# Performance work log

Hardware: AMD Instinct MI355X
Metric: run time of the kernel (lower is better)

## Reference

```python
import jax, jax.numpy as jnp
import numpy as np

N = 10000          # total nodes
N_AGENTS = 5000    # drones (x[:, -1] < 0)
E = 160000         # random edges (self-loops added in reference)
C_IN, H, C_HID, C_OUT = 16, 8, 128, 8
NEG_SLOPE = 0.2    # GATv2Conv default leaky_relu slope


def setup_inputs() -> dict:
    key = jax.random.key(0)
    ks = jax.random.split(key, 12)
    x = jax.random.normal(ks[0], (N, C_IN), dtype=jnp.float32)
    # last feature column encodes node type: <0 -> drone, >=0 -> goal
    type_col = jnp.where(jnp.arange(N) < N_AGENTS, -1.0, 1.0).astype(jnp.float32)
    x = x.at[:, -1].set(type_col)
    edge_index = jax.random.randint(ks[1], (2, E), 0, N, dtype=jnp.int32)
    s = 0.1  # glorot-ish scale
    return {
        "x": x,
        "edge_index": edge_index,
        "Wl1": s * jax.random.normal(ks[2], (C_IN, H * C_HID), jnp.float32),
        "bl1": jnp.zeros((H * C_HID,), jnp.float32),
        "Wr1": s * jax.random.normal(ks[3], (C_IN, H * C_HID), jnp.float32),
        "br1": jnp.zeros((H * C_HID,), jnp.float32),
        "att1": s * jax.random.normal(ks[4], (H, C_HID), jnp.float32),
        "b1": jnp.zeros((C_HID,), jnp.float32),
        "Wl2": s * jax.random.normal(ks[5], (C_HID, H * C_HID), jnp.float32),
        "bl2": jnp.zeros((H * C_HID,), jnp.float32),
        "Wr2": s * jax.random.normal(ks[6], (C_HID, H * C_HID), jnp.float32),
        "br2": jnp.zeros((H * C_HID,), jnp.float32),
        "att2": s * jax.random.normal(ks[7], (H, C_HID), jnp.float32),
        "b2": jnp.zeros((C_HID,), jnp.float32),
        "Wlin": s * jax.random.normal(ks[8], (C_HID, C_OUT), jnp.float32),
        "blin": jnp.zeros((C_OUT,), jnp.float32),
    }


def gatv2_conv(x, src, dst, Wl, bl, Wr, br, att, bias):
    """PyG GATv2Conv, heads=H, concat=False (head-mean), add_self_loops handled by caller."""
    n = x.shape[0]
    xl = (x @ Wl + bl).reshape(n, H, -1)   # [N,H,C] source transform
    xr = (x @ Wr + br).reshape(n, H, -1)   # [N,H,C] target transform
    e = jax.nn.leaky_relu(xl[src] + xr[dst], NEG_SLOPE)          # [E,H,C]
    alpha = jnp.einsum("ehc,hc->eh", e, att)                      # [E,H]
    # per-destination softmax over incoming edges
    m = jax.ops.segment_max(alpha, dst, num_segments=n)
    a = jnp.exp(alpha - m[dst])
    denom = jax.ops.segment_sum(a, dst, num_segments=n)
    a = a / (denom[dst] + 1e-16)
    out = jax.ops.segment_sum(xl[src] * a[:, :, None], dst, num_segments=n)  # [N,H,C]
    return out.mean(axis=1) + bias  # concat=False -> mean over heads


def reference(x, edge_index, Wl1, bl1, Wr1, br1, att1, b1,
              Wl2, bl2, Wr2, br2, att2, b2, Wlin, blin):
    n = x.shape[0]
    loops = jnp.arange(n, dtype=edge_index.dtype)
    src = jnp.concatenate([edge_index[0], loops])
    dst = jnp.concatenate([edge_index[1], loops])
    drone_mask = x[:, -1] < 0
    y = x  # bounds is None -> no division
    h = jax.nn.relu(gatv2_conv(y, src, dst, Wl1, bl1, Wr1, br1, att1, b1))
    h = jax.nn.relu(gatv2_conv(h, src, dst, Wl2, bl2, Wr2, br2, att2, b2))
    out = h @ Wlin + blin  # [N, C_OUT]
    idx = jnp.nonzero(drone_mask, size=N_AGENTS)[0]
    return out[idx]  # [N_AGENTS, C_OUT]
```

## Files before the change

kernel.cpp:

```cpp
#include <hip/hip_runtime.h>
#include <hip/hip_fp16.h>
#include <math.h>

#define N_NODES 10000
#define N_EDGES 160000
#define NAG     5000
#define HC      1024
#define CH      128
#define NEG     0.2f
#define BCAP    64

#define NSCAT   625
#define NGEMM   1256

typedef _Float16 f16x8 __attribute__((ext_vector_type(8)));
typedef _Float16 f16x2 __attribute__((ext_vector_type(2)));
typedef float f32x4 __attribute__((ext_vector_type(4)));

__device__ __forceinline__ __half2 pk_max(__half2 a, __half2 b) {
    __half2 r;
    asm volatile("v_pk_max_f16 %0, %1, %2" : "=v"(r) : "v"(a), "v"(b));
    return r;
}

__device__ __forceinline__ void edge_accum(float4 raw, const __half2* xr2, const __half2* att2,
                                           float& lsum, float* acc, bool valid) {
    __half2* hp = (__half2*)&raw;
    const __half2 neg2 = __float2half2_rn(NEG);
    float p = 0.f;
    #pragma unroll
    for (int j = 0; j < 4; j++) {
        __half2 z = __hadd2(hp[j], xr2[j]);
        __half2 lz = pk_max(z, __hmul2(z, neg2));
#if __has_builtin(__builtin_amdgcn_fdot2)
        p = __builtin_amdgcn_fdot2(*(f16x2*)&lz, *(const f16x2*)&att2[j], p, false);
#else
        float2 lf = __half22float2(lz);
        float2 af = __half22float2(att2[j]);
        p = fmaf(lf.x, af.x, p);
        p = fmaf(lf.y, af.y, p);
#endif
    }
    p += __shfl_xor(p, 1, 64);
    p += __shfl_xor(p, 2, 64);
    p += __shfl_xor(p, 4, 64);
    p += __shfl_xor(p, 8, 64);
    float w = valid ? __expf(p) : 0.f;
    lsum += w;
    #pragma unroll
    for (int j = 0; j < 4; j++) {
        acc[2 * j]     = fmaf(__low2float(hp[j]),  w, acc[2 * j]);
        acc[2 * j + 1] = fmaf(__high2float(hp[j]), w, acc[2 * j + 1]);
    }
}

template <int K, int KA, bool TRANS, typename AT>
__device__ void gemm_tile(char* smem, int vt,
                          const AT* __restrict__ A, const float* __restrict__ tb,
                          const _Float16* __restrict__ Whl, const float* __restrict__ bl,
                          const _Float16* __restrict__ Whr, const float* __restrict__ br,
                          _Float16* __restrict__ xl, _Float16* __restrict__ xr,
                          int limitL, int limitR) {
    _Float16* ash = (_Float16*)smem;
    float (*eps)[68] = (float(*)[68])smem;
    __shared__ float bsh[256];
    const int AS = K + 8;
    int by = vt & 7;
    int rowblk = (vt >> 3) * 64;
    bool right = by >= 4;
    if (rowblk >= (right ? limitR : limitL)) return;
    const _Float16* Wh = right ? Whr : Whl;
    const float* bs    = right ? br : bl;
    _Float16* outp     = right ? xr : xl;
    int colbase = (by & 3) * 256;
    int t = threadIdx.x;
    int w = t >> 6, l = t & 63;
    int m = l & 15, q = l >> 4;

    bsh[t] = bs[colbase + t];
    for (int idx = t; idx < 64 * (K / 8); idx += 256) {
        int r  = idx / (K / 8);
        int c8 = (idx % (K / 8)) * 8;
        int row = rowblk + r;
        f16x8 hv = (f16x8){0, 0, 0, 0, 0, 0, 0, 0};
        if (row < N_NODES && c8 < KA) {
            if constexpr (TRANS) {
                f16x8 hvv[8];
                #pragma unroll
                for (int h = 0; h < 8; h++)
                    hvv[h] = *(const f16x8*)((const _Float16*)A + (size_t)row * HC + h * CH + c8);
                #pragma unroll
                for (int j = 0; j < 8; j++) {
                    float s = 0.f;
                    #pragma unroll
                    for (int h = 0; h < 8; h++) s += (float)hvv[h][j];
                    hv[j] = (_Float16)fmaxf(fmaf(s, 0.125f, tb[c8 + j]), 0.f);
                }
            } else if constexpr (sizeof(AT) == 2) {
                hv = *(const f16x8*)((const _Float16*)A + (size_t)row * KA + c8);
            } else {
                float4 v0 = *(const float4*)((const float*)A + (size_t)row * KA + c8);
                float4 v1 = *(const float4*)((const float*)A + (size_t)row * KA + c8 + 4);
                hv[0] = (_Float16)v0.x; hv[1] = (_Float16)v0.y; hv[2] = (_Float16)v0.z; hv[3] = (_Float16)v0.w;
                hv[4] = (_Float16)v1.x; hv[5] = (_Float16)v1.y; hv[6] = (_Float16)v1.z; hv[7] = (_Float16)v1.w;
            }
        }
        *(f16x8*)&ash[r * AS + c8] = hv;
    }
    __syncthreads();

    f32x4 acc[16];
    #pragma unroll
    for (int i = 0; i < 16; i++) acc[i] = (f32x4){0.f, 0.f, 0.f, 0.f};

    #pragma unroll
    for (int kq = 0; kq < K / 32; kq++) {
        f16x8 af = *(const f16x8*)&ash[(w * 16 + m) * AS + kq * 32 + q * 8];
        const _Float16* base = Wh + (((size_t)(kq * 64 + (colbase >> 4))) << 9) + l * 8;
        #pragma unroll
        for (int tile = 0; tile < 16; tile++) {
            f16x8 bf = *(const f16x8*)(base + ((size_t)tile << 9));
            acc[tile] = __builtin_amdgcn_mfma_f32_16x16x32_f16(af, bf, acc[tile], 0, 0, 0);
        }
    }

    float bv[16];
    #pragma unroll
    for (int tile = 0; tile < 16; tile++) bv[tile] = bsh[tile * 16 + m];

    for (int cgk = 0; cgk < 4; cgk++) {
        __syncthreads();
        #pragma unroll
        for (int tt = 0; tt < 4; tt++) {
            int tile = cgk * 4 + tt;
            int cl = tt * 16 + m;
            #pragma unroll
            for (int reg = 0; reg < 4; reg++)
                eps[w * 16 + q * 4 + reg][cl] = acc[tile][reg] + bv[tile];
        }
        __syncthreads();
        int colg = colbase + cgk * 64;
        int cc = (t & 15) * 4;
        #pragma unroll
        for (int it = 0; it < 4; it++) {
            int r = it * 16 + (t >> 4);
            int row = rowblk + r;
            if (row < N_NODES) {
                float4 v = *(const float4*)&eps[r][cc];
                __half2 h01 = __floats2half2_rn(v.x, v.y);
                __half2 h23 = __floats2half2_rn(v.z, v.w);
                float2 st;
                st.x = *(float*)&h01;
                st.y = *(float*)&h23;
                *(float2*)(outp + (size_t)row * HC + colg + cc) = st;
            }
        }
    }
}

__global__ __launch_bounds__(64) void gat_kernel(const __half* __restrict__ xl,
                                                 const _Float16* __restrict__ xr,
                                                 const float* __restrict__ att,
                                                 const int* __restrict__ cnt,
                                                 const int* __restrict__ srcs,
                                                 _Float16* __restrict__ hpart) {
    int b = blockIdx.x;
    int dst = b >> 3, head = b & 7;
    int t = threadIdx.x;
    int slot = t >> 4, l16 = t & 15;
    int ch0 = head * CH + l16 * 8;

    __half2 xr2[4], att2[4];
    {
        f16x8 xv = *(const f16x8*)(xr + (size_t)dst * HC + ch0);
        __half2* xp = (__half2*)&xv;
        xr2[0] = xp[0]; xr2[1] = xp[1]; xr2[2] = xp[2]; xr2[3] = xp[3];
        float4 b0 = *(const float4*)(att + ch0);
        float4 b1 = *(const float4*)(att + ch0 + 4);
        att2[0] = __floats2half2_rn(b0.x, b0.y);
        att2[1] = __floats2half2_rn(b0.z, b0.w);
        att2[2] = __floats2half2_rn(b1.x, b1.y);
        att2[3] = __floats2half2_rn(b1.z, b1.w);
    }

    float acc[8];
    #pragma unroll
    for (int j = 0; j < 8; j++) acc[j] = 0.f;
    float lsum = 0.f;

    int e0 = dst << 6;
    int e1 = e0 + cnt[dst];
    for (int base = e0; base < e1; base += 4) {
        int ee = base + slot;
        bool valid = ee < e1;
        int s = srcs[valid ? ee : e0];
        float4 raw = *(const float4*)(xl + (size_t)s * HC + ch0);
        edge_accum(raw, xr2, att2, lsum, acc, valid);
    }

    #pragma unroll
    for (int j = 0; j < 8; j++) {
        acc[j] += __shfl_xor(acc[j], 16, 64);
        acc[j] += __shfl_xor(acc[j], 32, 64);
    }
    lsum += __shfl_xor(lsum, 16, 64);
    lsum += __shfl_xor(lsum, 32, 64);

    if (t < 16) {
        float inv = 1.f / (lsum + 1e-16f);
        f16x8 hv;
        #pragma unroll
        for (int j = 0; j < 8; j++) hv[j] = (_Float16)(acc[j] * inv);
        *(f16x8*)(hpart + (size_t)dst * HC + head * CH + l16 * 8) = hv;
    }
}

__global__ __launch_bounds__(256) void out_kernel(const _Float16* __restrict__ hpart2,
                                                  const float* __restrict__ b2,
                                                  const float* __restrict__ Wlin,
                                                  const float* __restrict__ blin,
                                                  float* __restrict__ out) {
    int dst = blockIdx.x;
    int t = threadIdx.x;
    __shared__ float hrow[CH];
    if (t < 128) {
        float s = 0.f;
        #pragma unroll
        for (int h = 0; h < 8; h++) s += (float)hpart2[(size_t)dst * HC + h * CH + t];
        hrow[t] = fmaxf(fmaf(s, 0.125f, b2[t]), 0.f);
    }
    __syncthreads();
    if (t < 64) {
        int j = t & 7, p8 = t >> 3;
        float v = 0.f;
        #pragma unroll
        for (int kk = 0; kk < 16; kk++) {
            int k = p8 * 16 + kk;
            v = fmaf(hrow[k], Wlin[k * 8 + j], v);
        }
        v += __shfl_xor(v, 8, 64);
        v += __shfl_xor(v, 16, 64);
        v += __shfl_xor(v, 32, 64);
        if (t < 8) out[(size_t)dst * 8 + t] = v + blin[t];
    }
}

__device__ __forceinline__ void emit_frag8(const float* __restrict__ W, _Float16* __restrict__ o,
                                           int tid, int KAreal) {
    int f = tid >> 6, l = tid & 63;
    int kq = f >> 6, tile = f & 63;
    int m = l & 15, q = l >> 4;
    int col = tile * 16 + m;
    float v[8];
    #pragma unroll
    for (int j = 0; j < 8; j++) {
        int k = kq * 32 + q * 8 + j;
        v[j] = (k < KAreal) ? W[k * 1024 + col] : 0.f;
    }
    f16x8 hv;
    #pragma unroll
    for (int j = 0; j < 8; j++) hv[j] = (_Float16)v[j];
    *(f16x8*)(o + ((size_t)tid << 3)) = hv;
}

__global__ __launch_bounds__(256) void prep_kernel(const float* __restrict__ Wl1, const float* __restrict__ Wr1,
                                                   const float* __restrict__ Wl2, const float* __restrict__ Wr2,
                                                   _Float16* __restrict__ w1l, _Float16* __restrict__ w1r,
                                                   _Float16* __restrict__ w2l, _Float16* __restrict__ w2r,
                                                   int* __restrict__ cnt, int* __restrict__ srcs) {
    int t = threadIdx.x;
    int b = blockIdx.x;
    if (b < 40) {
        int i = b * 256 + t;
        if (i < N_NODES) {
            cnt[i] = 1;
            srcs[i << 6] = i;
        }
        return;
    }
    if (b < 72) {
        int tid = (b - 40) * 256 + t;
        if (tid < 4096) emit_frag8(Wl1, w1l, tid, 16);
        else            emit_frag8(Wr1, w1r, tid - 4096, 16);
        return;
    }
    int tid = (b - 72) * 256 + t;
    if (tid < 16384) emit_frag8(Wl2, w2l, tid, 128);
    else             emit_frag8(Wr2, w2r, tid - 16384, 128);
}

__global__ __launch_bounds__(256) void d2_kernel(const int* __restrict__ esrc,
                                                 const int* __restrict__ edst,
                                                 int* __restrict__ cnt,
                                                 int* __restrict__ srcs,
                                                 const float* __restrict__ x,
                                                 const _Float16* __restrict__ w1l, const float* __restrict__ bl1,
                                                 const _Float16* __restrict__ w1r, const float* __restrict__ br1,
                                                 _Float16* __restrict__ xlh, _Float16* __restrict__ xrh) {
    __shared__ __align__(16) char smem[17408];
    int b = blockIdx.x;
    if (b < NGEMM) {
        gemm_tile<32, 16, false, float>(smem, b, x, nullptr, w1l, bl1, w1r, br1,
                                        xlh, xrh, N_NODES, N_NODES);
    } else {
        int e = (b - NGEMM) * 256 + threadIdx.x;
        int d = edst[e];
        int p = atomicAdd(&cnt[d], 1);
        if (p < BCAP) srcs[(d << 6) + p] = esrc[e];
    }
}

__global__ __launch_bounds__(256) void gemm2_kernel(const _Float16* __restrict__ hpart1,
                                                    const float* __restrict__ b1,
                                                    const _Float16* __restrict__ w2l, const float* __restrict__ bl2,
                                                    const _Float16* __restrict__ w2r, const float* __restrict__ br2,
                                                    _Float16* __restrict__ xlh, _Float16* __restrict__ xrh) {
    __shared__ __align__(16) char smem[17408];
    gemm_tile<128, 128, true, _Float16>(smem, blockIdx.x, hpart1, b1, w2l, bl2, w2r, br2,
                                        xlh, xrh, N_NODES, NAG);
}

extern "C" void kernel_launch(void* const* d_in, const int* in_sizes, int n_in,
                              void* d_out, int out_size, void* d_ws, size_t ws_size,
                              hipStream_t stream) {
    const float* x    = (const float*)d_in[0];
    const int*   ei   = (const int*)d_in[1];
    const float* Wl1  = (const float*)d_in[2];
    const float* bl1  = (const float*)d_in[3];
    const float* Wr1  = (const float*)d_in[4];
    const float* br1  = (const float*)d_in[5];
    const float* att1 = (const float*)d_in[6];
    const float* b1   = (const float*)d_in[7];
    const float* Wl2  = (const float*)d_in[8];
    const float* bl2  = (const float*)d_in[9];
    const float* Wr2  = (const float*)d_in[10];
    const float* br2  = (const float*)d_in[11];
    const float* att2 = (const float*)d_in[12];
    const float* b2   = (const float*)d_in[13];
    const float* Wlin = (const float*)d_in[14];
    const float* blin = (const float*)d_in[15];
    float* out = (float*)d_out;

    const int* esrc = ei;
    const int* edst = ei + N_EDGES;

    char* p = (char*)d_ws;
    __half* xlh    = (__half*)p;               p += (size_t)N_NODES * HC * sizeof(__half);
    _Float16* xrh  = (_Float16*)p;             p += (size_t)N_NODES * HC * sizeof(_Float16);
    _Float16* hp1  = (_Float16*)p;             p += (size_t)N_NODES * HC * sizeof(_Float16);
    _Float16* hp2  = (_Float16*)p;             p += (size_t)NAG * HC * sizeof(_Float16);
    _Float16* w1l = (_Float16*)p;              p += 1024 * 32 * sizeof(_Float16);
    _Float16* w1r = (_Float16*)p;              p += 1024 * 32 * sizeof(_Float16);
    _Float16* w2l = (_Float16*)p;              p += 1024 * 128 * sizeof(_Float16);
    _Float16* w2r = (_Float16*)p;              p += 1024 * 128 * sizeof(_Float16);
    int* cnt  = (int*)p;                       p += (size_t)N_NODES * sizeof(int) + 64;
    int* srcs = (int*)p;

    prep_kernel<<<200, 256, 0, stream>>>(Wl1, Wr1, Wl2, Wr2, w1l, w1r, w2l, w2r, cnt, srcs);
    d2_kernel<<<NGEMM + NSCAT, 256, 0, stream>>>(esrc, edst, cnt, srcs, x,
                                                 w1l, bl1, w1r, br1,
                                                 (_Float16*)xlh, xrh);
    gat_kernel<<<N_NODES * 8, 64, 0, stream>>>(xlh, xrh, att1, cnt, srcs, hp1);
    gemm2_kernel<<<NGEMM, 256, 0, stream>>>(hp1, b1, w2l, bl2, w2r, br2,
                                            (_Float16*)xlh, xrh);
    gat_kernel<<<NAG * 8, 64, 0, stream>>>(xlh, xrh, att2, cnt, srcs, hp2);
    out_kernel<<<NAG, 256, 0, stream>>>(hp2, b2, Wlin, blin, out);
}
```

Baseline: 234.1 us.

## Use persistent grid-stride GAT blocks, split head-mean fold out of GEMM2, use fma_mix

The GAT kernels now launch a fixed number of block groups that loop over destination nodes with a grid stride, instead of one block per destination and head. This cuts block launch overhead and keeps the attention vector loaded across nodes. The head-mean, bias and relu fold moves out of the GEMM2 A-tile load into a separate fold kernel that writes a compact 128-wide fp16 matrix. GEMM2 no longer re-reduces the 8 heads in every column tile, at the cost of one extra launch and a round trip through memory. The edge accumulate now uses v_fma_mix_f32 so the half-to-float convert is folded into the FMA.

```diff
diff --git a/kernel.cpp b/kernel.cpp
--- a/kernel.cpp
+++ b/kernel.cpp
@@ -12,6 +12,8 @@
 
 #define NSCAT   625
 #define NGEMM   1256
+#define GATG1   2048
+#define GATG2   1024
 
 typedef _Float16 f16x8 __attribute__((ext_vector_type(8)));
 typedef _Float16 f16x2 __attribute__((ext_vector_type(2)));
@@ -49,14 +51,16 @@
     lsum += w;
     #pragma unroll
     for (int j = 0; j < 4; j++) {
-        acc[2 * j]     = fmaf(__low2float(hp[j]),  w, acc[2 * j]);
-        acc[2 * j + 1] = fmaf(__high2float(hp[j]), w, acc[2 * j + 1]);
-    }
-}
-
-template <int K, int KA, bool TRANS, typename AT>
+        asm("v_fma_mix_f32 %0, %1, %2, %0 op_sel_hi:[1,0,0]"
+            : "+v"(acc[2 * j]) : "v"(hp[j]), "v"(w));
+        asm("v_fma_mix_f32 %0, %1, %2, %0 op_sel:[1,0,0] op_sel_hi:[1,0,0]"
+            : "+v"(acc[2 * j + 1]) : "v"(hp[j]), "v"(w));
+    }
+}
+
+template <int K, int KA, typename AT>
 __device__ void gemm_tile(char* smem, int vt,
-                          const AT* __restrict__ A, const float* __restrict__ tb,
+                          const AT* __restrict__ A,
                           const _Float16* __restrict__ Whl, const float* __restrict__ bl,
                           const _Float16* __restrict__ Whr, const float* __restrict__ br,
                           _Float16* __restrict__ xl, _Float16* __restrict__ xr,
@@ -84,19 +88,7 @@
         int row = rowblk + r;
         f16x8 hv = (f16x8){0, 0, 0, 0, 0, 0, 0, 0};
         if (row < N_NODES && c8 < KA) {
-            if constexpr (TRANS) {
-                f16x8 hvv[8];
-                #pragma unroll
-                for (int h = 0; h < 8; h++)
-                    hvv[h] = *(const f16x8*)((const _Float16*)A + (size_t)row * HC + h * CH + c8);
-                #pragma unroll
-                for (int j = 0; j < 8; j++) {
-                    float s = 0.f;
-                    #pragma unroll
-                    for (int h = 0; h < 8; h++) s += (float)hvv[h][j];
-                    hv[j] = (_Float16)fmaxf(fmaf(s, 0.125f, tb[c8 + j]), 0.f);
-                }
-            } else if constexpr (sizeof(AT) == 2) {
+            if constexpr (sizeof(AT) == 2) {
                 hv = *(const f16x8*)((const _Float16*)A + (size_t)row * KA + c8);
             } else {
                 float4 v0 = *(const float4*)((const float*)A + (size_t)row * KA + c8);
@@ -163,18 +155,16 @@
                                                  const float* __restrict__ att,
                                                  const int* __restrict__ cnt,
                                                  const int* __restrict__ srcs,
-                                                 _Float16* __restrict__ hpart) {
+                                                 _Float16* __restrict__ hpart,
+                                                 int ngroups, int ndst) {
     int b = blockIdx.x;
-    int dst = b >> 3, head = b & 7;
+    int g = b >> 3, head = b & 7;
     int t = threadIdx.x;
     int slot = t >> 4, l16 = t & 15;
     int ch0 = head * CH + l16 * 8;
 
-    __half2 xr2[4], att2[4];
+    __half2 att2[4];
     {
-        f16x8 xv = *(const f16x8*)(xr + (size_t)dst * HC + ch0);
-        __half2* xp = (__half2*)&xv;
-        xr2[0] = xp[0]; xr2[1] = xp[1]; xr2[2] = xp[2]; xr2[3] = xp[3];
         float4 b0 = *(const float4*)(att + ch0);
         float4 b1 = *(const float4*)(att + ch0 + 4);
         att2[0] = __floats2half2_rn(b0.x, b0.y);
@@ -183,36 +173,70 @@
         att2[3] = __floats2half2_rn(b1.z, b1.w);
     }
 
-    float acc[8];
-    #pragma unroll
-    for (int j = 0; j < 8; j++) acc[j] = 0.f;
-    float lsum = 0.f;
-
-    int e0 = dst << 6;
-    int e1 = e0 + cnt[dst];
-    for (int base = e0; base < e1; base += 4) {
-        int ee = base + slot;
-        bool valid = ee < e1;
-        int s = srcs[valid ? ee : e0];
-        float4 raw = *(const float4*)(xl + (size_t)s * HC + ch0);
-        edge_accum(raw, xr2, att2, lsum, acc, valid);
-    }
-
+    for (int dst = g; dst < ndst; dst += ngroups) {
+        __half2 xr2[4];
+        {
+            f16x8 xv = *(const f16x8*)(xr + (size_t)dst * HC + ch0);
+            __half2* xp = (__half2*)&xv;
+            xr2[0] = xp[0]; xr2[1] = xp[1]; xr2[2] = xp[2]; xr2[3] = xp[3];
+        }
+
+        float acc[8];
+        #pragma unroll
+        for (int j = 0; j < 8; j++) acc[j] = 0.f;
+        float lsum = 0.f;
+
+        int e0 = dst << 6;
+        int e1 = e0 + cnt[dst];
+        for (int base = e0; base < e1; base += 4) {
+            int ee = base + slot;
+            bool valid = ee < e1;
+            int s = srcs[valid ? ee : e0];
+            float4 raw = *(const float4*)(xl + (size_t)s * HC + ch0);
+            edge_accum(raw, xr2, att2, lsum, acc, valid);
+        }
+
+        #pragma unroll
+        for (int j = 0; j < 8; j++) {
+            acc[j] += __shfl_xor(acc[j], 16, 64);
+            acc[j] += __shfl_xor(acc[j], 32, 64);
+        }
+        lsum += __shfl_xor(lsum, 16, 64);
+        lsum += __shfl_xor(lsum, 32, 64);
+
+        if (t < 16) {
+            float inv = 1.f / (lsum + 1e-16f);
+            f16x8 hv;
+            #pragma unroll
+            for (int j = 0; j < 8; j++) hv[j] = (_Float16)(acc[j] * inv);
+            *(f16x8*)(hpart + (size_t)dst * HC + head * CH + l16 * 8) = hv;
+        }
+    }
+}
+
+__global__ __launch_bounds__(256) void fold_kernel(const _Float16* __restrict__ hpart,
+                                                   const float* __restrict__ b1,
+                                                   _Float16* __restrict__ h1c) {
+    int t = threadIdx.x;
+    int row = blockIdx.x * 16 + (t >> 4);
+    int ch0 = (t & 15) * 8;
+    if (row >= N_NODES) return;
+    f16x8 hvv[8];
+    #pragma unroll
+    for (int h = 0; h < 8; h++)
+        hvv[h] = *(const f16x8*)(hpart + (size_t)row * HC + h * CH + ch0);
+    float4 bb0 = *(const float4*)(b1 + ch0);
+    float4 bb1 = *(const float4*)(b1 + ch0 + 4);
+    float tb[8] = {bb0.x, bb0.y, bb0.z, bb0.w, bb1.x, bb1.y, bb1.z, bb1.w};
+    f16x8 o;
     #pragma unroll
     for (int j = 0; j < 8; j++) {
-        acc[j] += __shfl_xor(acc[j], 16, 64);
-        acc[j] += __shfl_xor(acc[j], 32, 64);
-    }
-    lsum += __shfl_xor(lsum, 16, 64);
-    lsum += __shfl_xor(lsum, 32, 64);
-
-    if (t < 16) {
-        float inv = 1.f / (lsum + 1e-16f);
-        f16x8 hv;
-        #pragma unroll
-        for (int j = 0; j < 8; j++) hv[j] = (_Float16)(acc[j] * inv);
-        *(f16x8*)(hpart + (size_t)dst * HC + head * CH + l16 * 8) = hv;
-    }
+        float s = 0.f;
+        #pragma unroll
+        for (int h = 0; h < 8; h++) s += (float)hvv[h][j];
+        o[j] = (_Float16)fmaxf(fmaf(s, 0.125f, tb[j]), 0.f);
+    }
+    *(f16x8*)(h1c + (size_t)row * CH + ch0) = o;
 }
 
 __global__ __launch_bounds__(256) void out_kernel(const _Float16* __restrict__ hpart2,
@@ -300,8 +324,8 @@
     __shared__ __align__(16) char smem[17408];
     int b = blockIdx.x;
     if (b < NGEMM) {
-        gemm_tile<32, 16, false, float>(smem, b, x, nullptr, w1l, bl1, w1r, br1,
-                                        xlh, xrh, N_NODES, N_NODES);
+        gemm_tile<32, 16, float>(smem, b, x, w1l, bl1, w1r, br1,
+                                 xlh, xrh, N_NODES, N_NODES);
     } else {
         int e = (b - NGEMM) * 256 + threadIdx.x;
         int d = edst[e];
@@ -310,14 +334,13 @@
     }
 }
 
-__global__ __launch_bounds__(256) void gemm2_kernel(const _Float16* __restrict__ hpart1,
-                                                    const float* __restrict__ b1,
+__global__ __launch_bounds__(256) void gemm2_kernel(const _Float16* __restrict__ h1c,
                                                     const _Float16* __restrict__ w2l, const float* __restrict__ bl2,
                                                     const _Float16* __restrict__ w2r, const float* __restrict__ br2,
                                                     _Float16* __restrict__ xlh, _Float16* __restrict__ xrh) {
     __shared__ __align__(16) char smem[17408];
-    gemm_tile<128, 128, true, _Float16>(smem, blockIdx.x, hpart1, b1, w2l, bl2, w2r, br2,
-                                        xlh, xrh, N_NODES, NAG);
+    gemm_tile<128, 128, _Float16>(smem, blockIdx.x, h1c, w2l, bl2, w2r, br2,
+                                  xlh, xrh, N_NODES, NAG);
 }
 
 extern "C" void kernel_launch(void* const* d_in, const int* in_sizes, int n_in,
@@ -349,6 +372,7 @@
     _Float16* xrh  = (_Float16*)p;             p += (size_t)N_NODES * HC * sizeof(_Float16);
     _Float16* hp1  = (_Float16*)p;             p += (size_t)N_NODES * HC * sizeof(_Float16);
     _Float16* hp2  = (_Float16*)p;             p += (size_t)NAG * HC * sizeof(_Float16);
+    _Float16* h1c  = (_Float16*)p;             p += (size_t)N_NODES * CH * sizeof(_Float16);
     _Float16* w1l = (_Float16*)p;              p += 1024 * 32 * sizeof(_Float16);
     _Float16* w1r = (_Float16*)p;              p += 1024 * 32 * sizeof(_Float16);
     _Float16* w2l = (_Float16*)p;              p += 1024 * 128 * sizeof(_Float16);
@@ -360,9 +384,12 @@
     d2_kernel<<<NGEMM + NSCAT, 256, 0, stream>>>(esrc, edst, cnt, srcs, x,
                                                  w1l, bl1, w1r, br1,
                                                  (_Float16*)xlh, xrh);
-    gat_kernel<<<N_NODES * 8, 64, 0, stream>>>(xlh, xrh, att1, cnt, srcs, hp1);
-    gemm2_kernel<<<NGEMM, 256, 0, stream>>>(hp1, b1, w2l, bl2, w2r, br2,
+    gat_kernel<<<GATG1 * 8, 64, 0, stream>>>(xlh, xrh, att1, cnt, srcs, hp1,
+                                             GATG1, N_NODES);
+    fold_kernel<<<(N_NODES + 15) / 16, 256, 0, stream>>>(hp1, b1, h1c);
+    gemm2_kernel<<<NGEMM, 256, 0, stream>>>(h1c, w2l, bl2, w2r, br2,
                                             (_Float16*)xlh, xrh);
-    gat_kernel<<<NAG * 8, 64, 0, stream>>>(xlh, xrh, att2, cnt, srcs, hp2);
+    gat_kernel<<<GATG2 * 8, 64, 0, stream>>>(xlh, xrh, att2, cnt, srcs, hp2,
+                                             GATG2, NAG);
     out_kernel<<<NAG, 256, 0, stream>>>(hp2, b2, Wlin, blin, out);
 }
```

New measurement: 220.6 us. 1.06x faster.
